# Optimization experiments

Measured on AMD Instinct MI355X. Metric: run time of the kernel, lower is better.

Reference implementation:

```python
import jax, jax.numpy as jnp
import numpy as np

B, S, D_IN, D_H = 4, 2048, 1024, 1024

def setup_inputs() -> dict:
    key = jax.random.key(0)
    kx, kq, kk, kv = jax.random.split(key, 4)
    # nn.Linear default init: U(-1/sqrt(fan_in), 1/sqrt(fan_in)); stored as [out, in]
    bound = 1.0 / np.sqrt(D_IN)
    x = jax.random.normal(kx, (B, S, D_IN), dtype=jnp.float32)
    W_q = jax.random.uniform(kq, (D_H, D_IN), jnp.float32, -bound, bound)
    W_k = jax.random.uniform(kk, (D_H, D_IN), jnp.float32, -bound, bound)
    W_v = jax.random.uniform(kv, (D_H, D_IN), jnp.float32, -bound, bound)
    return {"x": x, "W_q": W_q, "W_k": W_k, "W_v": W_v}

def reference(x, W_q, W_k, W_v):
    # Q = x @ W_q.T, etc. (nn.Linear with bias=False)
    Q = jnp.einsum('bsd,hd->bsh', x, W_q)
    K = jnp.einsum('bsd,hd->bsh', x, W_k)
    V = jnp.einsum('bsd,hd->bsh', x, W_v)
    # NOTE: original scales by sqrt(Q.shape[1]) == sqrt(seq_len), not sqrt(d)
    scale = 1.0 / jnp.sqrt(jnp.asarray(Q.shape[1], Q.dtype))
    scores = jnp.einsum('bqh,bkh->bqk', Q, K) * scale  # [B,S,S]
    attn = jax.nn.softmax(scores, axis=-1)
    return jnp.einsum('bqk,bkh->bqh', attn, V)
```

## Files before the change

kernel.cpp:

```cpp
#include <hip/hip_runtime.h>

typedef unsigned short ushort_t;
typedef __attribute__((ext_vector_type(8))) __bf16 bf16x8;
typedef __attribute__((ext_vector_type(4))) float floatx4;

__device__ __forceinline__ ushort_t f2bf(float f) {
    unsigned int u = __builtin_bit_cast(unsigned int, f);
    u = (u + 0x7fffu + ((u >> 16) & 1u)) >> 16;
    return (ushort_t)u;
}

__device__ __forceinline__ void async16(const ushort_t* g, ushort_t* l) {
    __builtin_amdgcn_global_load_lds(
        (const __attribute__((address_space(1))) unsigned int*)g,
        (__attribute__((address_space(3))) unsigned int*)l,
        16 , 0 , 0 );
}

__device__ __forceinline__ int sw(int row, int cg) {
    return ((row << 2) + ((cg ^ row ^ (row >> 2)) & 3)) << 3;
}

template <int BM, int BN, int IM, int IN>
__device__ __forceinline__ void gemm_core_p3(
    const ushort_t* __restrict__ A, int lda,
    const ushort_t* __restrict__ B, int ldb,
    int K, int tile_m, int tile_n,
    ushort_t* buf,
    floatx4 (&acc)[IM][IN]) {

    constexpr int SA = BM * 4 / 256;
    constexpr int SB = BN * 4 / 256;
    constexpr int SLOT = (BM + BN) * 32;
    constexpr int BOFF = BM * 32;

    const int tid  = threadIdx.x;
    const int lane = tid & 63;
    const int wave = tid >> 6;
    const int wm   = wave >> 1, wn = wave & 1;
    const int quad = lane >> 4;
    const int l16  = lane & 15;

#pragma unroll
    for (int i = 0; i < IM; i++)
#pragma unroll
        for (int j = 0; j < IN; j++) acc[i][j] = (floatx4){0.f, 0.f, 0.f, 0.f};

    const ushort_t* ga[SA];
    int la[SA];
#pragma unroll
    for (int s = 0; s < SA; s++) {
        int seg = tid + s * 256;
        int r = seg >> 2, c = (seg ^ r ^ (r >> 2)) & 3;
        ga[s] = A + (long)(r + tile_m) * lda + c * 8;
        la[s] = seg * 8;
    }
    const ushort_t* gb[SB];
    int lb[SB];
#pragma unroll
    for (int s = 0; s < SB; s++) {
        int seg = tid + s * 256;
        int r = seg >> 2, c = (seg ^ r ^ (r >> 2)) & 3;
        gb[s] = B + (long)(r + tile_n) * ldb + c * 8;
        lb[s] = BOFF + seg * 8;
    }

    const int nk = K >> 5;

#pragma unroll
    for (int p = 0; p < 2; ++p) {
#pragma unroll
        for (int s = 0; s < SA; s++) async16(ga[s] + p * 32, buf + p * SLOT + la[s]);
#pragma unroll
        for (int s = 0; s < SB; s++) async16(gb[s] + p * 32, buf + p * SLOT + lb[s]);
    }

    int slot = 0, slot2 = 2;
    for (int k = 0; k < nk; ++k) {
        if (k + 1 < nk) {
            if constexpr (SA + SB == 4)
                asm volatile("s_waitcnt vmcnt(4)" ::: "memory");
            else
                asm volatile("s_waitcnt vmcnt(2)" ::: "memory");
        } else {
            asm volatile("s_waitcnt vmcnt(0)" ::: "memory");
        }
        __builtin_amdgcn_s_barrier();
        asm volatile("" ::: "memory");

        if (k + 2 < nk) {
            const int koff = (k + 2) << 5;
            ushort_t* dst = buf + slot2 * SLOT;
#pragma unroll
            for (int s = 0; s < SA; s++) async16(ga[s] + koff, dst + la[s]);
#pragma unroll
            for (int s = 0; s < SB; s++) async16(gb[s] + koff, dst + lb[s]);
        }

        const ushort_t* as = buf + slot * SLOT;
        const ushort_t* bs = as + BOFF;
        bf16x8 af[IM], bfr[IN];
#pragma unroll
        for (int im = 0; im < IM; im++)
            af[im] = *(const bf16x8*)&as[sw(wm * IM * 16 + im * 16 + l16, quad)];
#pragma unroll
        for (int in = 0; in < IN; in++)
            bfr[in] = *(const bf16x8*)&bs[sw(wn * IN * 16 + in * 16 + l16, quad)];
#pragma unroll
        for (int im = 0; im < IM; im++)
#pragma unroll
            for (int in = 0; in < IN; in++)
                acc[im][in] = __builtin_amdgcn_mfma_f32_16x16x32_bf16(
                    af[im], bfr[in], acc[im][in], 0, 0, 0);

        slot  = (slot == 2) ? 0 : slot + 1;
        slot2 = (slot2 == 2) ? 0 : slot2 + 1;
    }
}

__global__ void cvt_kernel(const float* __restrict__ x,
                           const float* __restrict__ wv,
                           ushort_t* __restrict__ xb,
                           ushort_t* __restrict__ wvb,
                           float* __restrict__ lsum) {
    const int bx = blockIdx.x;
    if (bx >= 9216) {
        int idx = (bx - 9216) * 256 + threadIdx.x;
        ((float4*)lsum)[idx] = (float4){0.f, 0.f, 0.f, 0.f};
        return;
    }
    const float* src;
    ushort_t* dst;
    long g;
    if (bx < 8192) { src = x;  dst = xb;  g = ((long)bx * 256 + threadIdx.x) * 4; }
    else           { src = wv; dst = wvb; g = ((long)(bx - 8192) * 256 + threadIdx.x) * 4; }
    float4 v = *(const float4*)(src + g);
    ushort4 o;
    o.x = f2bf(v.x); o.y = f2bf(v.y); o.z = f2bf(v.z); o.w = f2bf(v.w);
    *(ushort4*)(dst + g) = o;
}

__global__ void tkern(const float* __restrict__ wq, const float* __restrict__ wk,
                      ushort_t* __restrict__ wqT, ushort_t* __restrict__ wkT) {
    const float* src = blockIdx.z ? wk : wq;
    ushort_t* dst = blockIdx.z ? wkT : wqT;
    __shared__ ushort_t tile[64 * 80];

    const int t = threadIdx.x;
    const int h0 = blockIdx.y * 64, d0 = blockIdx.x * 64;
    {
        int i = t >> 2, cg = (t & 3) << 4;
        const float4* p = (const float4*)(src + (long)(h0 + i) * 1024 + d0 + cg);
#pragma unroll
        for (int k = 0; k < 4; k++) {
            float4 v = p[k];
            ushort_t* q = &tile[i * 80 + cg + k * 4];
            q[0] = f2bf(v.x); q[1] = f2bf(v.y); q[2] = f2bf(v.z); q[3] = f2bf(v.w);
        }
    }
    __syncthreads();
    {
        int j = t >> 2, ig = (t & 3) << 4;
        ushort_t tmp[16];
#pragma unroll
        for (int k = 0; k < 16; k++) tmp[k] = tile[(ig + k) * 80 + j];
        ushort_t* o = dst + (long)(d0 + j) * 1024 + h0 + ig;
        *(uint4*)o = ((uint4*)tmp)[0];
        *(uint4*)(o + 8) = ((uint4*)tmp)[1];
    }
}

__global__ __launch_bounds__(256) void ggemm_kernel(
    const ushort_t* __restrict__ wkT, const ushort_t* __restrict__ wqT,
    ushort_t* __restrict__ G) {
    __shared__ __align__(16) ushort_t buf[3 * 128 * 32];
    const int tile_m = blockIdx.y * 64, tile_n = blockIdx.x * 64;
    floatx4 acc[2][2];
    gemm_core_p3<64, 64, 2, 2>(wkT, 1024, wqT, 1024, 1024, tile_m, tile_n, buf, acc);
    const int lane = threadIdx.x & 63, wave = threadIdx.x >> 6;
    const int wm = wave >> 1, wn = wave & 1, quad = lane >> 4, l16 = lane & 15;
#pragma unroll
    for (int im = 0; im < 2; im++)
#pragma unroll
        for (int r = 0; r < 4; r++) {
            int row = tile_m + wm * 32 + im * 16 + quad * 4 + r;
#pragma unroll
            for (int in = 0; in < 2; in++) {
                int col = tile_n + wn * 32 + in * 16 + l16;
                G[(long)row * 1024 + col] = f2bf(acc[im][in][r]);
            }
        }
}

__global__ __launch_bounds__(256) void yv_kernel(
    const ushort_t* __restrict__ xb,
    const ushort_t* __restrict__ Gb,
    const ushort_t* __restrict__ wvb,
    ushort_t* __restrict__ Yb,
    ushort_t* __restrict__ VTb) {

    __shared__ __align__(16) ushort_t buf[3 * 256 * 32];

    const int z = blockIdx.z;
    const ushort_t *A, *B;
    ushort_t* C;
    int ldc, tile_m, tile_n;
    if (z == 0) {
        A = xb; B = Gb; C = Yb; ldc = 1024;
        tile_m = blockIdx.y * 128; tile_n = blockIdx.x * 128;
    } else {
        A = wvb; B = xb; C = VTb; ldc = 8192;
        tile_m = blockIdx.x * 128; tile_n = blockIdx.y * 128;
    }

    floatx4 acc[4][4];
    gemm_core_p3<128, 128, 4, 4>(A, 1024, B, 1024, 1024, tile_m, tile_n, buf, acc);

    const int lane = threadIdx.x & 63, wave = threadIdx.x >> 6;
    const int wm = wave >> 1, wn = wave & 1, quad = lane >> 4, l16 = lane & 15;
#pragma unroll
    for (int im = 0; im < 4; im++)
#pragma unroll
        for (int r = 0; r < 4; r++) {
            int row = tile_m + wm * 64 + im * 16 + quad * 4 + r;
#pragma unroll
            for (int in = 0; in < 4; in++) {
                int col = tile_n + wn * 64 + in * 16 + l16;
                C[(long)row * ldc + col] = f2bf(acc[im][in][r]);
            }
        }
}

__global__ __launch_bounds__(256) void pexp_kernel(
    const ushort_t* __restrict__ Yb,
    const ushort_t* __restrict__ xb,
    ushort_t* __restrict__ Pb,
    float* __restrict__ lsum) {

    __shared__ __align__(16) ushort_t buf[3 * 256 * 32];

    const int z = blockIdx.z;
    const ushort_t* A = Yb + (long)z * 2097152;
    const ushort_t* B = xb + (long)z * 2097152;
    ushort_t* C = Pb + (long)z * 4194304;
    float* l = lsum + z * 2048;
    const int tile_m = blockIdx.y * 128;
    const int tile_n = blockIdx.x * 128;

    floatx4 acc[4][4];
    gemm_core_p3<128, 128, 4, 4>(A, 1024, B, 1024, 1024, tile_m, tile_n, buf, acc);

    const float scale = 0.022097086912079608f;
    const int lane = threadIdx.x & 63, wave = threadIdx.x >> 6;
    const int wm = wave >> 1, wn = wave & 1, quad = lane >> 4, l16 = lane & 15;
#pragma unroll
    for (int im = 0; im < 4; im++)
#pragma unroll
        for (int r = 0; r < 4; r++) {
            int row = tile_m + wm * 64 + im * 16 + quad * 4 + r;
            float psum = 0.f;
#pragma unroll
            for (int in = 0; in < 4; in++) {
                int col = tile_n + wn * 64 + in * 16 + l16;
                float e = __expf(acc[im][in][r] * scale);
                C[(long)row * 2048 + col] = f2bf(e);
                psum += e;
            }
            psum += __shfl_xor(psum, 1, 64);
            psum += __shfl_xor(psum, 2, 64);
            psum += __shfl_xor(psum, 4, 64);
            psum += __shfl_xor(psum, 8, 64);
            if (l16 == 0) atomicAdd(&l[row], psum);
        }
}

__global__ __launch_bounds__(256) void out_kernel(
    const ushort_t* __restrict__ Pb,
    const ushort_t* __restrict__ VTb,
    float* __restrict__ out,
    const float* __restrict__ lsum) {

    __shared__ __align__(16) ushort_t buf[3 * 256 * 32];

    const int z = blockIdx.z;
    const ushort_t* A = Pb + (long)z * 4194304;
    const ushort_t* B = VTb + (long)z * 2048;
    float* C = out + (long)z * 2097152;
    const float* l = lsum + z * 2048;
    const int tile_m = blockIdx.y * 128;
    const int tile_n = blockIdx.x * 128;

    floatx4 acc[4][4];
    gemm_core_p3<128, 128, 4, 4>(A, 2048, B, 8192, 2048, tile_m, tile_n, buf, acc);

    const int lane = threadIdx.x & 63, wave = threadIdx.x >> 6;
    const int wm = wave >> 1, wn = wave & 1, quad = lane >> 4, l16 = lane & 15;
#pragma unroll
    for (int im = 0; im < 4; im++)
#pragma unroll
        for (int r = 0; r < 4; r++) {
            int row = tile_m + wm * 64 + im * 16 + quad * 4 + r;
            float li = 1.0f / l[row];
#pragma unroll
            for (int in = 0; in < 4; in++) {
                int col = tile_n + wn * 64 + in * 16 + l16;
                C[(long)row * 1024 + col] = acc[im][in][r] * li;
            }
        }
}

extern "C" void kernel_launch(void* const* d_in, const int* in_sizes, int n_in,
                              void* d_out, int out_size, void* d_ws, size_t ws_size,
                              hipStream_t stream) {
    const float* x  = (const float*)d_in[0];
    const float* wq = (const float*)d_in[1];
    const float* wk = (const float*)d_in[2];
    const float* wv = (const float*)d_in[3];

    ushort_t* xb  = (ushort_t*)d_ws;
    ushort_t* wvb = xb  + 8388608;
    ushort_t* wqT = wvb + 1048576;
    ushort_t* wkT = wqT + 1048576;
    ushort_t* Gb  = wkT + 1048576;
    ushort_t* Yb  = Gb  + 1048576;
    ushort_t* VTb = Yb  + 8388608;
    ushort_t* Pb  = VTb + 8388608;
    float*    lsum = (float*)(Pb + 16777216);
    float*    out  = (float*)d_out;

    cvt_kernel<<<9224, 256, 0, stream>>>(x, wv, xb, wvb, lsum);

    tkern<<<dim3(16, 16, 2), 256, 0, stream>>>(wq, wk, wqT, wkT);

    ggemm_kernel<<<dim3(16, 16), 256, 0, stream>>>(wkT, wqT, Gb);

    yv_kernel<<<dim3(8, 64, 2), 256, 0, stream>>>(xb, Gb, wvb, Yb, VTb);

    pexp_kernel<<<dim3(16, 16, 4), 256, 0, stream>>>(Yb, xb, Pb, lsum);

    out_kernel<<<dim3(8, 16, 4), 256, 0, stream>>>(Pb, VTb, out, lsum);
}
```

Measured before the change: 243.9 us.

## Fuse prep kernels, co-schedule G and V GEMMs, use 256x128 eight-wave tiles

Merges the bf16 conversion, lsum zeroing and weight transpose into one prep launch. Computes G and V^T together in one 512-thread launch so the small G GEMM no longer runs alone ahead of them, and moves Y into its own kernel. The shared GEMM core gains a wave-count parameter, and the V^T and score/exp GEMMs move to 256x128 tiles with 8 waves to get more reuse per LDS stage. The cost is larger LDS use per block, tighter register limits from the launch bounds, and uneven work across blocks in the merged kernel.

```diff
diff --git a/kernel.cpp b/kernel.cpp
--- a/kernel.cpp
+++ b/kernel.cpp
@@ -21,7 +21,7 @@
     return ((row << 2) + ((cg ^ row ^ (row >> 2)) & 3)) << 3;
 }
 
-template <int BM, int BN, int IM, int IN>
+template <int BM, int BN, int IM, int IN, int NW>
 __device__ __forceinline__ void gemm_core_p3(
     const ushort_t* __restrict__ A, int lda,
     const ushort_t* __restrict__ B, int ldb,
@@ -29,8 +29,9 @@
     ushort_t* buf,
     floatx4 (&acc)[IM][IN]) {
 
-    constexpr int SA = BM * 4 / 256;
-    constexpr int SB = BN * 4 / 256;
+    constexpr int NT = NW * 64;
+    constexpr int SA = BM * 4 / NT;
+    constexpr int SB = BN * 4 / NT;
     constexpr int SLOT = (BM + BN) * 32;
     constexpr int BOFF = BM * 32;
 
@@ -50,7 +51,7 @@
     int la[SA];
 #pragma unroll
     for (int s = 0; s < SA; s++) {
-        int seg = tid + s * 256;
+        int seg = tid + s * NT;
         int r = seg >> 2, c = (seg ^ r ^ (r >> 2)) & 3;
         ga[s] = A + (long)(r + tile_m) * lda + c * 8;
         la[s] = seg * 8;
@@ -59,7 +60,7 @@
     int lb[SB];
 #pragma unroll
     for (int s = 0; s < SB; s++) {
-        int seg = tid + s * 256;
+        int seg = tid + s * NT;
         int r = seg >> 2, c = (seg ^ r ^ (r >> 2)) & 3;
         gb[s] = B + (long)(r + tile_n) * ldb + c * 8;
         lb[s] = BOFF + seg * 8;
@@ -80,6 +81,8 @@
         if (k + 1 < nk) {
             if constexpr (SA + SB == 4)
                 asm volatile("s_waitcnt vmcnt(4)" ::: "memory");
+            else if constexpr (SA + SB == 3)
+                asm volatile("s_waitcnt vmcnt(3)" ::: "memory");
             else
                 asm volatile("s_waitcnt vmcnt(2)" ::: "memory");
         } else {
@@ -118,36 +121,40 @@
     }
 }
 
-__global__ void cvt_kernel(const float* __restrict__ x,
-                           const float* __restrict__ wv,
-                           ushort_t* __restrict__ xb,
-                           ushort_t* __restrict__ wvb,
-                           float* __restrict__ lsum) {
+__global__ void prep_kernel(const float* __restrict__ x,
+                            const float* __restrict__ wq,
+                            const float* __restrict__ wk,
+                            const float* __restrict__ wv,
+                            ushort_t* __restrict__ xb,
+                            ushort_t* __restrict__ wvb,
+                            ushort_t* __restrict__ wqT,
+                            ushort_t* __restrict__ wkT,
+                            float* __restrict__ lsum) {
     const int bx = blockIdx.x;
-    if (bx >= 9216) {
-        int idx = (bx - 9216) * 256 + threadIdx.x;
+    const int t = threadIdx.x;
+    if (bx < 9216) {
+        const float* src;
+        ushort_t* dst;
+        long g;
+        if (bx < 8192) { src = x;  dst = xb;  g = ((long)bx * 256 + t) * 4; }
+        else           { src = wv; dst = wvb; g = ((long)(bx - 8192) * 256 + t) * 4; }
+        float4 v = *(const float4*)(src + g);
+        ushort4 o;
+        o.x = f2bf(v.x); o.y = f2bf(v.y); o.z = f2bf(v.z); o.w = f2bf(v.w);
+        *(ushort4*)(dst + g) = o;
+        return;
+    }
+    if (bx < 9224) {
+        int idx = (bx - 9216) * 256 + t;
         ((float4*)lsum)[idx] = (float4){0.f, 0.f, 0.f, 0.f};
         return;
     }
-    const float* src;
-    ushort_t* dst;
-    long g;
-    if (bx < 8192) { src = x;  dst = xb;  g = ((long)bx * 256 + threadIdx.x) * 4; }
-    else           { src = wv; dst = wvb; g = ((long)(bx - 8192) * 256 + threadIdx.x) * 4; }
-    float4 v = *(const float4*)(src + g);
-    ushort4 o;
-    o.x = f2bf(v.x); o.y = f2bf(v.y); o.z = f2bf(v.z); o.w = f2bf(v.w);
-    *(ushort4*)(dst + g) = o;
-}
-
-__global__ void tkern(const float* __restrict__ wq, const float* __restrict__ wk,
-                      ushort_t* __restrict__ wqT, ushort_t* __restrict__ wkT) {
-    const float* src = blockIdx.z ? wk : wq;
-    ushort_t* dst = blockIdx.z ? wkT : wqT;
+    const int tt = bx - 9224;
+    const float* src = (tt >= 256) ? wk : wq;
+    ushort_t* dst = (tt >= 256) ? wkT : wqT;
+    const int id = tt & 255;
+    const int h0 = (id >> 4) * 64, d0 = (id & 15) * 64;
     __shared__ ushort_t tile[64 * 80];
-
-    const int t = threadIdx.x;
-    const int h0 = blockIdx.y * 64, d0 = blockIdx.x * 64;
     {
         int i = t >> 2, cg = (t & 3) << 4;
         const float4* p = (const float4*)(src + (long)(h0 + i) * 1024 + d0 + cg);
@@ -170,51 +177,29 @@
     }
 }
 
-__global__ __launch_bounds__(256) void ggemm_kernel(
+__global__ __launch_bounds__(512, 4) void gv_kernel(
     const ushort_t* __restrict__ wkT, const ushort_t* __restrict__ wqT,
-    ushort_t* __restrict__ G) {
-    __shared__ __align__(16) ushort_t buf[3 * 128 * 32];
-    const int tile_m = blockIdx.y * 64, tile_n = blockIdx.x * 64;
-    floatx4 acc[2][2];
-    gemm_core_p3<64, 64, 2, 2>(wkT, 1024, wqT, 1024, 1024, tile_m, tile_n, buf, acc);
-    const int lane = threadIdx.x & 63, wave = threadIdx.x >> 6;
-    const int wm = wave >> 1, wn = wave & 1, quad = lane >> 4, l16 = lane & 15;
-#pragma unroll
-    for (int im = 0; im < 2; im++)
-#pragma unroll
-        for (int r = 0; r < 4; r++) {
-            int row = tile_m + wm * 32 + im * 16 + quad * 4 + r;
-#pragma unroll
-            for (int in = 0; in < 2; in++) {
-                int col = tile_n + wn * 32 + in * 16 + l16;
-                G[(long)row * 1024 + col] = f2bf(acc[im][in][r]);
-            }
-        }
-}
-
-__global__ __launch_bounds__(256) void yv_kernel(
-    const ushort_t* __restrict__ xb,
-    const ushort_t* __restrict__ Gb,
-    const ushort_t* __restrict__ wvb,
-    ushort_t* __restrict__ Yb,
-    ushort_t* __restrict__ VTb) {
-
-    __shared__ __align__(16) ushort_t buf[3 * 256 * 32];
-
-    const int z = blockIdx.z;
+    const ushort_t* __restrict__ wvb, const ushort_t* __restrict__ xb,
+    ushort_t* __restrict__ Gb, ushort_t* __restrict__ VTb) {
+
+    __shared__ __align__(16) ushort_t buf[3 * 384 * 32];
+
     const ushort_t *A, *B;
     ushort_t* C;
     int ldc, tile_m, tile_n;
-    if (z == 0) {
-        A = xb; B = Gb; C = Yb; ldc = 1024;
-        tile_m = blockIdx.y * 128; tile_n = blockIdx.x * 128;
+    if (blockIdx.x < 32) {
+        A = wkT; B = wqT; C = Gb; ldc = 1024;
+        tile_m = (blockIdx.x >> 3) * 256;
+        tile_n = (blockIdx.x & 7) * 128;
     } else {
+        int id = blockIdx.x - 32;
         A = wvb; B = xb; C = VTb; ldc = 8192;
-        tile_m = blockIdx.x * 128; tile_n = blockIdx.y * 128;
+        tile_m = (id >> 6) * 256;
+        tile_n = (id & 63) * 128;
     }
 
     floatx4 acc[4][4];
-    gemm_core_p3<128, 128, 4, 4>(A, 1024, B, 1024, 1024, tile_m, tile_n, buf, acc);
+    gemm_core_p3<256, 128, 4, 4, 8>(A, 1024, B, 1024, 1024, tile_m, tile_n, buf, acc);
 
     const int lane = threadIdx.x & 63, wave = threadIdx.x >> 6;
     const int wm = wave >> 1, wn = wave & 1, quad = lane >> 4, l16 = lane & 15;
@@ -231,24 +216,51 @@
         }
 }
 
-__global__ __launch_bounds__(256) void pexp_kernel(
+__global__ __launch_bounds__(256) void y_kernel(
+    const ushort_t* __restrict__ xb,
+    const ushort_t* __restrict__ Gb,
+    ushort_t* __restrict__ Yb) {
+
+    __shared__ __align__(16) ushort_t buf[3 * 256 * 32];
+    const int tile_m = blockIdx.y * 128;
+    const int tile_n = blockIdx.x * 128;
+
+    floatx4 acc[4][4];
+    gemm_core_p3<128, 128, 4, 4, 4>(xb, 1024, Gb, 1024, 1024, tile_m, tile_n, buf, acc);
+
+    const int lane = threadIdx.x & 63, wave = threadIdx.x >> 6;
+    const int wm = wave >> 1, wn = wave & 1, quad = lane >> 4, l16 = lane & 15;
+#pragma unroll
+    for (int im = 0; im < 4; im++)
+#pragma unroll
+        for (int r = 0; r < 4; r++) {
+            int row = tile_m + wm * 64 + im * 16 + quad * 4 + r;
+#pragma unroll
+            for (int in = 0; in < 4; in++) {
+                int col = tile_n + wn * 64 + in * 16 + l16;
+                Yb[(long)row * 1024 + col] = f2bf(acc[im][in][r]);
+            }
+        }
+}
+
+__global__ __launch_bounds__(512, 4) void pexp_kernel(
     const ushort_t* __restrict__ Yb,
     const ushort_t* __restrict__ xb,
     ushort_t* __restrict__ Pb,
     float* __restrict__ lsum) {
 
-    __shared__ __align__(16) ushort_t buf[3 * 256 * 32];
+    __shared__ __align__(16) ushort_t buf[3 * 384 * 32];
 
     const int z = blockIdx.z;
     const ushort_t* A = Yb + (long)z * 2097152;
     const ushort_t* B = xb + (long)z * 2097152;
     ushort_t* C = Pb + (long)z * 4194304;
     float* l = lsum + z * 2048;
-    const int tile_m = blockIdx.y * 128;
+    const int tile_m = blockIdx.y * 256;
     const int tile_n = blockIdx.x * 128;
 
     floatx4 acc[4][4];
-    gemm_core_p3<128, 128, 4, 4>(A, 1024, B, 1024, 1024, tile_m, tile_n, buf, acc);
+    gemm_core_p3<256, 128, 4, 4, 8>(A, 1024, B, 1024, 1024, tile_m, tile_n, buf, acc);
 
     const float scale = 0.022097086912079608f;
     const int lane = threadIdx.x & 63, wave = threadIdx.x >> 6;
@@ -291,7 +303,7 @@
     const int tile_n = blockIdx.x * 128;
 
     floatx4 acc[4][4];
-    gemm_core_p3<128, 128, 4, 4>(A, 2048, B, 8192, 2048, tile_m, tile_n, buf, acc);
+    gemm_core_p3<128, 128, 4, 4, 4>(A, 2048, B, 8192, 2048, tile_m, tile_n, buf, acc);
 
     const int lane = threadIdx.x & 63, wave = threadIdx.x >> 6;
     const int wm = wave >> 1, wn = wave & 1, quad = lane >> 4, l16 = lane & 15;
@@ -328,15 +340,13 @@
     float*    lsum = (float*)(Pb + 16777216);
     float*    out  = (float*)d_out;
 
-    cvt_kernel<<<9224, 256, 0, stream>>>(x, wv, xb, wvb, lsum);
-
-    tkern<<<dim3(16, 16, 2), 256, 0, stream>>>(wq, wk, wqT, wkT);
-
-    ggemm_kernel<<<dim3(16, 16), 256, 0, stream>>>(wkT, wqT, Gb);
-
-    yv_kernel<<<dim3(8, 64, 2), 256, 0, stream>>>(xb, Gb, wvb, Yb, VTb);
-
-    pexp_kernel<<<dim3(16, 16, 4), 256, 0, stream>>>(Yb, xb, Pb, lsum);
+    prep_kernel<<<9736, 256, 0, stream>>>(x, wq, wk, wv, xb, wvb, wqT, wkT, lsum);
+
+    gv_kernel<<<288, 512, 0, stream>>>(wkT, wqT, wvb, xb, Gb, VTb);
+
+    y_kernel<<<dim3(8, 64), 256, 0, stream>>>(xb, Gb, Yb);
+
+    pexp_kernel<<<dim3(16, 8, 4), 512, 0, stream>>>(Yb, xb, Pb, lsum);
 
     out_kernel<<<dim3(8, 16, 4), 256, 0, stream>>>(Pb, VTb, out, lsum);
 }
```

Result: faster. 238.1 us (-2.4%).
